# Kernel optimization log

Measured on AMD Instinct MI355X. Metric: run time of the kernel, lower is better.

Reference implementation:

```python
import jax, jax.numpy as jnp
import numpy as np

H = 8  # attention heads
L = 2  # transformer layers


def conv1d(x, w, b=None, pad=0, dil=1):
    # x: (B, Cin, T), w: (Cout, Cin, K)
    y = jax.lax.conv_general_dilated(x, w, window_strides=(1,), padding=[(pad, pad)],
                                     rhs_dilation=(dil,), dimension_numbers=('NCH', 'OIH', 'NCH'))
    if b is not None:
        y = y + b[None, :, None]
    return y


def bn1d(x, p, eps=1e-5):
    # eval-mode BatchNorm1d; p: (4, C) = [gamma, beta, running_mean, running_var]
    g, b, m, v = p
    return g[None, :, None] * (x - m[None, :, None]) * jax.lax.rsqrt(v + eps)[None, :, None] + b[None, :, None]


def layernorm(x, g, b, eps=1e-5):
    m = x.mean(-1, keepdims=True)
    v = ((x - m) ** 2).mean(-1, keepdims=True)
    return (x - m) * jax.lax.rsqrt(v + eps) * g + b


def mha(x, in_w, in_b, out_w, out_b):
    # x: (T, B, E) seq-first, like nn.MultiheadAttention (eval, no dropout)
    T, B, E = x.shape
    dh = E // H
    qkv = x @ in_w.T + in_b
    q, k, v = jnp.split(qkv, 3, axis=-1)
    sh = lambda a: a.reshape(T, B, H, dh).transpose(1, 2, 0, 3)  # (B, H, T, dh)
    q, k, v = sh(q), sh(k), sh(v)
    attn = jax.nn.softmax(jnp.einsum('bhqd,bhkd->bhqk', q, k) * (dh ** -0.5), axis=-1)
    o = jnp.einsum('bhqk,bhkd->bhqd', attn, v).transpose(2, 0, 1, 3).reshape(T, B, E)
    return o @ out_w.T + out_b


def _forward(x, wts, cw1, cb1, bn1, cw2, cb2, bn2, cw3, cb3, bn3, cw4, cb4, bn4, cw5,
             tcw_in, tcb_in, t_in_w, t_in_b, t_out_w, t_out_b, ln1_g, ln1_b,
             ff_w1, ff_b1, ff_w2, ff_b2, ln2_g, ln2_b, tcw_out, tcb_out,
             cw6, bn6, bw1, bb1, bw2, bb2, bw3, bb3):
    out = x.transpose(0, 2, 1)  # (B, 2048, T)
    residual = out
    # multi-dilation conv branches: Conv1d -> ReLU -> BN
    o1 = bn1d(jax.nn.relu(conv1d(out, cw1, cb1, pad=1)), bn1)
    o2 = bn1d(jax.nn.relu(conv1d(out, cw2, cb2, pad=2, dil=2)), bn2)
    o3 = bn1d(jax.nn.relu(conv1d(out, cw3, cb3, pad=4, dil=4)), bn3)
    o4 = bn1d(jax.nn.relu(conv1d(out, cw4, cb4, pad=8, dil=4)), bn4)  # k=5, d=4, p=8
    out_d = wts[0] * o1 + wts[1] * o2 + wts[2] * o3 + wts[3] * o4  # (B, 512, T)
    # conv_5: 2048 -> 512, k=1, no bias
    out = jax.nn.relu(conv1d(out, cw5))
    # TransformerFeatureAggregator
    out = conv1d(out, tcw_in, tcb_in)  # 1x1 conv 512->512
    out = out.transpose(2, 0, 1)  # (T, B, 512)
    for i in range(L):
        a = mha(out, t_in_w[i], t_in_b[i], t_out_w[i], t_out_b[i])
        out = layernorm(out + a, ln1_g[i], ln1_b[i])
        ff = jax.nn.relu(out @ ff_w1[i].T + ff_b1[i]) @ ff_w2[i].T + ff_b2[i]
        out = layernorm(out + ff, ln2_g[i], ln2_b[i])
    out = out.transpose(1, 2, 0)  # (B, 512, T)
    out = conv1d(out, tcw_out, tcb_out)
    out = jnp.concatenate([out_d, out], axis=1)  # (B, 1024, T)
    out = bn1d(jax.nn.relu(conv1d(out, cw6, pad=1)), bn6)  # (B, 2048, T)
    # Bottleneck residual block
    r = out
    b = jax.nn.relu(conv1d(out, bw1, bb1))
    b = jax.nn.relu(conv1d(b, bw2, bb2, pad=1))
    b = conv1d(b, bw3, bb3)
    out = jax.nn.relu(b + r)
    out = out + residual
    return out.transpose(0, 2, 1)  # (B, T, 2048)


def setup_inputs() -> dict:
    key = jax.random.key(0)
    ks = iter(jax.random.split(key, 80))

    def rn(shape, s=0.02):
        return jax.random.normal(next(ks), shape, jnp.float32) * s

    def bn_p(c):
        return jnp.stack([1.0 + rn((c,), 0.1), rn((c,), 0.1), rn((c,), 0.1),
                          0.5 + jax.random.uniform(next(ks), (c,), jnp.float32)])

    B, T, D = 8, 1024, 2048
    return dict(
        x=jax.random.normal(next(ks), (B, T, D), jnp.float32),
        wts=jnp.ones((4,), jnp.float32),
        cw1=rn((512, D, 3)), cb1=rn((512,)), bn1=bn_p(512),
        cw2=rn((512, D, 3)), cb2=rn((512,)), bn2=bn_p(512),
        cw3=rn((512, D, 3)), cb3=rn((512,)), bn3=bn_p(512),
        cw4=rn((512, D, 5)), cb4=rn((512,)), bn4=bn_p(512),
        cw5=rn((512, D, 1)),
        tcw_in=rn((512, 512, 1)), tcb_in=rn((512,)),
        t_in_w=rn((L, 3 * 512, 512)), t_in_b=rn((L, 3 * 512)),
        t_out_w=rn((L, 512, 512)), t_out_b=rn((L, 512)),
        ln1_g=jnp.ones((L, 512), jnp.float32), ln1_b=jnp.zeros((L, 512), jnp.float32),
        ff_w1=rn((L, 2048, 512)), ff_b1=rn((L, 2048)),
        ff_w2=rn((L, 512, 2048)), ff_b2=rn((L, 512)),
        ln2_g=jnp.ones((L, 512), jnp.float32), ln2_b=jnp.zeros((L, 512), jnp.float32),
        tcw_out=rn((512, 512, 1)), tcb_out=rn((512,)),
        cw6=rn((2048, 1024, 3)), bn6=bn_p(2048),
        bw1=rn((512, 2048, 1)), bb1=rn((512,)),
        bw2=rn((512, 512, 3)), bb2=rn((512,)),
        bw3=rn((2048, 512, 1)), bb3=rn((2048,)),
    )


def reference(x, wts, cw1, cb1, bn1, cw2, cb2, bn2, cw3, cb3, bn3, cw4, cb4, bn4, cw5,
              tcw_in, tcb_in, t_in_w, t_in_b, t_out_w, t_out_b, ln1_g, ln1_b,
              ff_w1, ff_b1, ff_w2, ff_b2, ln2_g, ln2_b, tcw_out, tcb_out,
              cw6, bn6, bw1, bb1, bw2, bb2, bw3, bb3):
    return _forward(x, wts, cw1, cb1, bn1, cw2, cb2, bn2, cw3, cb3, bn3, cw4, cb4, bn4, cw5,
                    tcw_in, tcb_in, t_in_w, t_in_b, t_out_w, t_out_b, ln1_g, ln1_b,
                    ff_w1, ff_b1, ff_w2, ff_b2, ln2_g, ln2_b, tcw_out, tcb_out,
                    cw6, bn6, bw1, bb1, bw2, bb2, bw3, bb3)
```

## Files before the change

### kernel.cpp

```cpp
#include <hip/hip_runtime.h>
#include <hip/hip_bf16.h>


typedef __attribute__((ext_vector_type(4))) float f32x4;
typedef __attribute__((ext_vector_type(8))) short short8;
typedef __attribute__((ext_vector_type(8))) unsigned short ushort8;

__device__ __forceinline__ unsigned short f2bu(float f) {
    __hip_bfloat16 h = __float2bfloat16(f);
    return *reinterpret_cast<unsigned short*>(&h);
}
__device__ __forceinline__ float bu2f(unsigned short u) {
    __hip_bfloat16 h = *reinterpret_cast<__hip_bfloat16*>(&u);
    return __bfloat162float(h);
}

__device__ __forceinline__ void gload16(const void* g, void* l) {
    __builtin_amdgcn_global_load_lds(
        (const __attribute__((address_space(1))) unsigned int*)g,
        (__attribute__((address_space(3))) unsigned int*)l, 16, 0, 0);
}

__global__ void cast_kernel(const float* __restrict__ in, unsigned short* __restrict__ out, int n8)
{
    for (int i = blockIdx.x * blockDim.x + threadIdx.x; i < n8; i += gridDim.x * blockDim.x) {
        const float4* p = (const float4*)in + (size_t)i * 2;
        float4 a = p[0], b = p[1];
        ushort8 o;
        o[0] = f2bu(a.x); o[1] = f2bu(a.y); o[2] = f2bu(a.z); o[3] = f2bu(a.w);
        o[4] = f2bu(b.x); o[5] = f2bu(b.y); o[6] = f2bu(b.z); o[7] = f2bu(b.w);
        *(ushort8*)(out + (size_t)i * 8) = o;
    }
}

struct WJob { const float* src; unsigned short* dst; int N, K, taps; };
struct WJobs { WJob j[14]; int n; };

__global__ void wtrans_multi(WJobs jobs)
{
    for (int q = 0; q < jobs.n; ++q) {
        const float* __restrict__ src = jobs.j[q].src;
        unsigned short* __restrict__ dst = jobs.j[q].dst;
        const int N = jobs.j[q].N, K = jobs.j[q].K, taps = jobs.j[q].taps;
        const int total = N * K * taps;
        for (int idx = blockIdx.x * blockDim.x + threadIdx.x; idx < total;
             idx += gridDim.x * blockDim.x) {
            int i   = idx % K;
            int rem = idx / K;
            int o   = rem % N;
            int k   = rem / N;
            dst[idx] = f2bu(src[((size_t)o * K + i) * (size_t)taps + k]);
        }
    }
}

#define SKEY(r) (((r) >> 2) & 3)

template<int BM_, int EPI>
__global__ __launch_bounds__(256)
void mgemm(const __hip_bfloat16* __restrict__ A, int lda,
           const __hip_bfloat16* __restrict__ Bw, const float* __restrict__ bias,
           float* __restrict__ Cf, __hip_bfloat16* __restrict__ Cb, int ldc,
           int N, int K,
           const float* __restrict__ r1, int ldr, const float* __restrict__ r2)
{
    constexpr int MREP = BM_ / 32;
    __shared__ __align__(16) short As[2][BM_ * 32];
    __shared__ __align__(16) short Bs[2][128 * 32];

    const int tid  = threadIdx.x;
    const int w    = tid >> 6;
    const int lane = tid & 63;
    const int wr   = w >> 1, wc = w & 1;
    const int m_base = blockIdx.x * BM_;
    const int n_base = blockIdx.y * 128;
    const int lrr = lane >> 2;
    const int lj  = lane & 3;

    f32x4 acc[MREP][4];
#pragma unroll
    for (int m = 0; m < MREP; ++m)
#pragma unroll
        for (int n = 0; n < 4; ++n) acc[m][n] = (f32x4){0.f, 0.f, 0.f, 0.f};

    auto stage = [&](int nb, int kc) {
#pragma unroll
        for (int cb = 0; cb < 2; ++cb) {
            const int cc = w + cb * 4;
            const int r  = cc * 16 + lrr;
            const int jc = lj ^ SKEY(r);
            gload16((const void*)(Bw + (size_t)(n_base + r) * K + kc + jc * 8),
                    (void*)&Bs[nb][cc * 512]);
        }
#pragma unroll
        for (int ca = 0; ca < BM_ / 64; ++ca) {
            const int cc = w + ca * 4;
            const int r  = cc * 16 + lrr;
            const int jc = lj ^ SKEY(r);
            gload16((const void*)(A + (size_t)(m_base + r) * lda + kc + jc * 8),
                    (void*)&As[nb][cc * 512]);
        }
    };

    stage(0, 0);
    __syncthreads();
    int cur = 0;
    const int nt = K / 32;
    for (int t = 0; t < nt; ++t) {
        if (t + 1 < nt) stage(cur ^ 1, (t + 1) * 32);

        short8 a[MREP], b[4];
#pragma unroll
        for (int m = 0; m < MREP; ++m) {
            const int i = wr * (BM_ / 2) + m * 16 + (lane & 15);
            a[m] = *(const short8*)&As[cur][i * 32 + (((lane >> 4) ^ SKEY(i)) * 8)];
        }
#pragma unroll
        for (int n = 0; n < 4; ++n) {
            const int r = wc * 64 + n * 16 + (lane & 15);
            b[n] = *(const short8*)&Bs[cur][r * 32 + (((lane >> 4) ^ SKEY(r)) * 8)];
        }
#pragma unroll
        for (int m = 0; m < MREP; ++m)
#pragma unroll
            for (int n = 0; n < 4; ++n)
                acc[m][n] = __builtin_amdgcn_mfma_f32_16x16x32_bf16(a[m], b[n], acc[m][n], 0, 0, 0);

        __syncthreads();
        cur ^= 1;
    }

#pragma unroll
    for (int m = 0; m < MREP; ++m) {
#pragma unroll
        for (int n = 0; n < 4; ++n) {
#pragma unroll
            for (int j = 0; j < 4; ++j) {
                const int row = m_base + wr * (BM_ / 2) + m * 16 + (lane >> 4) * 4 + j;
                const int col = n_base + wc * 64 + n * 16 + (lane & 15);
                float v = acc[m][n][j];
                if (bias) v += bias[col];
                const size_t idx = (size_t)row * ldc + col;
                if (EPI == 1) v = fmaxf(v, 0.f);
                if (EPI == 3) {
                    v += r1[(size_t)row * ldr + col];
                    v = fmaxf(v, 0.f) + r2[(size_t)row * 2048 + col];
                    Cf[idx] = v;
                } else {
                    if (Cf) Cf[idx] = v;
                    if (Cb) Cb[idx] = __float2bfloat16(v);
                }
            }
        }
    }
}

template<int NTAPS, int EPI>
__global__ __launch_bounds__(256)
void cgemm(const __hip_bfloat16* __restrict__ A1, const __hip_bfloat16* __restrict__ A2,
           int split, int lda,
           const __hip_bfloat16* __restrict__ Bw, const float* __restrict__ bias,
           float* __restrict__ Cf, __hip_bfloat16* __restrict__ Cb, int ldc,
           int N, int K,
           int o0, int o1, int o2,
           const float* __restrict__ bnp,
           const __hip_bfloat16* __restrict__ zb)
{
    __shared__ __align__(16) short As[144 * 32];
    __shared__ __align__(16) short Bs[NTAPS * 128 * 32];

    const int tid  = threadIdx.x;
    const int w    = tid >> 6;
    const int lane = tid & 63;
    const int wr   = w >> 1, wc = w & 1;
    const int m_base = blockIdx.x * 128;
    const int n_base = blockIdx.y * 128;
    const int tb   = m_base & 1023;
    const int lrr  = lane >> 2;
    const int lj   = lane & 3;

    f32x4 acc[4][4];
#pragma unroll
    for (int m = 0; m < 4; ++m)
#pragma unroll
        for (int n = 0; n < 4; ++n) acc[m][n] = (f32x4){0.f, 0.f, 0.f, 0.f};

    for (int kc = 0; kc < K; kc += 32) {
        __syncthreads();
        for (int c = w; c < 9; c += 4) {
            const int i    = c * 16 + lrr;
            const int jc   = lj ^ SKEY(i);
            const int trow = tb + i - 8;
            const int c0   = kc + jc * 8;
            const void* src;
            if ((unsigned)trow < 1024u) {
                const int g = m_base - 8 + i;
                src = (c0 < split) ? (const void*)(A1 + (size_t)g * lda + c0)
                                   : (const void*)(A2 + (size_t)g * lda + (c0 - split));
            } else {
                src = (const void*)(zb + jc * 8);
            }
            gload16(src, (void*)&As[c * 512]);
        }
        for (int cb = w; cb < NTAPS * 8; cb += 4) {
            const int tap = cb >> 3, sub = cb & 7;
            const int r   = sub * 16 + lrr;
            const int jc  = lj ^ SKEY(r);
            gload16((const void*)(Bw + ((size_t)tap * N + n_base + r) * K + kc + jc * 8),
                    (void*)&Bs[cb * 512]);
        }
        __syncthreads();

#pragma unroll
        for (int tap = 0; tap < NTAPS; ++tap) {
            const int off = (tap == 0) ? o0 : (tap == 1) ? o1 : o2;
            short8 a[4], b[4];
#pragma unroll
            for (int m = 0; m < 4; ++m) {
                const int i = 8 + off + wr * 64 + m * 16 + (lane & 15);
                a[m] = *(const short8*)&As[i * 32 + (((lane >> 4) ^ SKEY(i)) * 8)];
            }
#pragma unroll
            for (int n = 0; n < 4; ++n) {
                const int r = wc * 64 + n * 16 + (lane & 15);
                b[n] = *(const short8*)&Bs[tap * 4096 + r * 32 + (((lane >> 4) ^ SKEY(r)) * 8)];
            }
#pragma unroll
            for (int m = 0; m < 4; ++m)
#pragma unroll
                for (int n = 0; n < 4; ++n)
                    acc[m][n] = __builtin_amdgcn_mfma_f32_16x16x32_bf16(a[m], b[n], acc[m][n], 0, 0, 0);
        }
    }

#pragma unroll
    for (int m = 0; m < 4; ++m) {
#pragma unroll
        for (int n = 0; n < 4; ++n) {
#pragma unroll
            for (int j = 0; j < 4; ++j) {
                const int row = m_base + wr * 64 + m * 16 + (lane >> 4) * 4 + j;
                const int col = n_base + wc * 64 + n * 16 + (lane & 15);
                float v = acc[m][n][j];
                if (bias) v += bias[col];
                const size_t idx = (size_t)row * ldc + col;
                if (EPI == 1) v = fmaxf(v, 0.f);
                if (EPI == 2) {
                    v = fmaxf(v, 0.f);
                    const float g  = bnp[col];
                    const float be = bnp[N + col];
                    const float mu = bnp[2 * N + col];
                    const float va = bnp[3 * N + col];
                    v = g * (v - mu) * rsqrtf(va + 1e-5f) + be;
                }
                if (Cf) Cf[idx] = v;
                if (Cb) Cb[idx] = __float2bfloat16(v);
            }
        }
    }
}

template<int NTAPS>
__global__ __launch_bounds__(512, 4)
void cgemm2(const __hip_bfloat16* __restrict__ A1, const __hip_bfloat16* __restrict__ A2,
            int split, int lda,
            const __hip_bfloat16* __restrict__ Bw, const float* __restrict__ bias,
            float* __restrict__ Cf, __hip_bfloat16* __restrict__ Cb, int ldc,
            int N, int K,
            int o0, int o1, int o2,
            const float* __restrict__ bnp,
            const __hip_bfloat16* __restrict__ zb)
{
    __shared__ __align__(16) short As[272 * 32];
    __shared__ __align__(16) short Bs[NTAPS * 128 * 32];

    const int tid  = threadIdx.x;
    const int w    = tid >> 6;
    const int lane = tid & 63;
    const int wr   = w >> 1, wc = w & 1;
    const int m_base = blockIdx.x * 256;
    const int n_base = blockIdx.y * 128;
    const int tb   = m_base & 1023;
    const int lrr  = lane >> 2;
    const int lj   = lane & 3;

    f32x4 acc[4][4];
#pragma unroll
    for (int m = 0; m < 4; ++m)
#pragma unroll
        for (int n = 0; n < 4; ++n) acc[m][n] = (f32x4){0.f, 0.f, 0.f, 0.f};

    for (int kc = 0; kc < K; kc += 32) {
        __syncthreads();
        for (int c = w; c < 17; c += 8) {
            const int i    = c * 16 + lrr;
            const int jc   = lj ^ SKEY(i);
            const int trow = tb + i - 8;
            const int c0   = kc + jc * 8;
            const void* src;
            if ((unsigned)trow < 1024u) {
                const int g = m_base - 8 + i;
                src = (c0 < split) ? (const void*)(A1 + (size_t)g * lda + c0)
                                   : (const void*)(A2 + (size_t)g * lda + (c0 - split));
            } else {
                src = (const void*)(zb + jc * 8);
            }
            gload16(src, (void*)&As[c * 512]);
        }
        for (int cb = w; cb < NTAPS * 8; cb += 8) {
            const int tap = cb >> 3, sub = cb & 7;
            const int r   = sub * 16 + lrr;
            const int jc  = lj ^ SKEY(r);
            gload16((const void*)(Bw + ((size_t)tap * N + n_base + r) * K + kc + jc * 8),
                    (void*)&Bs[cb * 512]);
        }
        __syncthreads();

#pragma unroll
        for (int tap = 0; tap < NTAPS; ++tap) {
            const int off = (tap == 0) ? o0 : (tap == 1) ? o1 : o2;
            short8 a[4], b[4];
#pragma unroll
            for (int m = 0; m < 4; ++m) {
                const int i = 8 + off + wr * 64 + m * 16 + (lane & 15);
                a[m] = *(const short8*)&As[i * 32 + (((lane >> 4) ^ SKEY(i)) * 8)];
            }
#pragma unroll
            for (int n = 0; n < 4; ++n) {
                const int r = wc * 64 + n * 16 + (lane & 15);
                b[n] = *(const short8*)&Bs[tap * 4096 + r * 32 + (((lane >> 4) ^ SKEY(r)) * 8)];
            }
#pragma unroll
            for (int m = 0; m < 4; ++m)
#pragma unroll
                for (int n = 0; n < 4; ++n)
                    acc[m][n] = __builtin_amdgcn_mfma_f32_16x16x32_bf16(a[m], b[n], acc[m][n], 0, 0, 0);
        }
    }

#pragma unroll
    for (int m = 0; m < 4; ++m) {
#pragma unroll
        for (int n = 0; n < 4; ++n) {
#pragma unroll
            for (int j = 0; j < 4; ++j) {
                const int row = m_base + wr * 64 + m * 16 + (lane >> 4) * 4 + j;
                const int col = n_base + wc * 64 + n * 16 + (lane & 15);
                float v = acc[m][n][j];
                if (bias) v += bias[col];
                v = fmaxf(v, 0.f);
                const float g  = bnp[col];
                const float be = bnp[N + col];
                const float mu = bnp[2 * N + col];
                const float va = bnp[3 * N + col];
                v = g * (v - mu) * rsqrtf(va + 1e-5f) + be;
                const size_t idx = (size_t)row * ldc + col;
                if (Cf) Cf[idx] = v;
                if (Cb) Cb[idx] = __float2bfloat16(v);
            }
        }
    }
}

struct BrP {
    const __hip_bfloat16* W;
    const float* bias;
    const float* bn;
    __hip_bfloat16* out;
    int ntaps;
    int o0, o1, o2, o3, o4;
};
struct BrPs { BrP p[5]; };

__global__ __launch_bounds__(512, 4)
void bgemm(const __hip_bfloat16* __restrict__ A, BrPs ps,
           const float* __restrict__ wts,
           const __hip_bfloat16* __restrict__ zb)
{
    __shared__ __align__(16) short As[272 * 32];
    __shared__ __align__(16) short Bs[5 * 128 * 32];

    const int tid  = threadIdx.x;
    const int w    = tid >> 6;
    const int lane = tid & 63;
    const int wr   = w >> 1, wc = w & 1;
    const int m_base = blockIdx.x * 256;
    const int n_base = blockIdx.y * 128;
    const int z    = blockIdx.z;
    const BrP p    = ps.p[z];
    const int tb   = m_base & 1023;
    const int lrr  = lane >> 2;
    const int lj   = lane & 3;
    const int ntaps = p.ntaps;

    f32x4 acc[4][4];
#pragma unroll
    for (int m = 0; m < 4; ++m)
#pragma unroll
        for (int n = 0; n < 4; ++n) acc[m][n] = (f32x4){0.f, 0.f, 0.f, 0.f};

    for (int kc = 0; kc < 2048; kc += 32) {
        __syncthreads();
        for (int c = w; c < 17; c += 8) {
            const int i    = c * 16 + lrr;
            const int jc   = lj ^ SKEY(i);
            const int trow = tb + i - 8;
            const void* src;
            if ((unsigned)trow < 1024u)
                src = (const void*)(A + (size_t)(m_base - 8 + i) * 2048 + kc + jc * 8);
            else
                src = (const void*)(zb + jc * 8);
            gload16(src, (void*)&As[c * 512]);
        }
        for (int cb = w; cb < ntaps * 8; cb += 8) {
            const int tap = cb >> 3, sub = cb & 7;
            const int r   = sub * 16 + lrr;
            const int jc  = lj ^ SKEY(r);
            gload16((const void*)(p.W + ((size_t)tap * 512 + n_base + r) * 2048 + kc + jc * 8),
                    (void*)&Bs[cb * 512]);
        }
        __syncthreads();

#pragma unroll 5
        for (int tap = 0; tap < ntaps; ++tap) {
            const int off = (tap == 0) ? p.o0 : (tap == 1) ? p.o1 : (tap == 2) ? p.o2
                          : (tap == 3) ? p.o3 : p.o4;
            short8 a[4], b[4];
#pragma unroll
            for (int m = 0; m < 4; ++m) {
                const int i = 8 + off + wr * 64 + m * 16 + (lane & 15);
                a[m] = *(const short8*)&As[i * 32 + (((lane >> 4) ^ SKEY(i)) * 8)];
            }
#pragma unroll
            for (int n = 0; n < 4; ++n) {
                const int r = wc * 64 + n * 16 + (lane & 15);
                b[n] = *(const short8*)&Bs[tap * 4096 + r * 32 + (((lane >> 4) ^ SKEY(r)) * 8)];
            }
#pragma unroll
            for (int m = 0; m < 4; ++m)
#pragma unroll
                for (int n = 0; n < 4; ++n)
                    acc[m][n] = __builtin_amdgcn_mfma_f32_16x16x32_bf16(a[m], b[n], acc[m][n], 0, 0, 0);
        }
    }

    const float wz = wts[z & 3];
#pragma unroll
    for (int m = 0; m < 4; ++m) {
#pragma unroll
        for (int n = 0; n < 4; ++n) {
#pragma unroll
            for (int j = 0; j < 4; ++j) {
                const int row = m_base + wr * 64 + m * 16 + (lane >> 4) * 4 + j;
                const int col = n_base + wc * 64 + n * 16 + (lane & 15);
                float v = acc[m][n][j];
                if (p.bias) v += p.bias[col];
                v = fmaxf(v, 0.f);
                if (p.bn) {
                    const float g  = p.bn[col];
                    const float be = p.bn[512 + col];
                    const float mu = p.bn[1024 + col];
                    const float va = p.bn[1536 + col];
                    v = (g * (v - mu) * rsqrtf(va + 1e-5f) + be) * wz;
                }
                p.out[(size_t)row * 512 + col] = __float2bfloat16(v);
            }
        }
    }
}

__global__ void bsum_kernel(const unsigned short* __restrict__ b0, const unsigned short* __restrict__ b1,
                            const unsigned short* __restrict__ b2, const unsigned short* __restrict__ b3,
                            unsigned short* __restrict__ o, int n8)
{
    for (int i = blockIdx.x * blockDim.x + threadIdx.x; i < n8; i += gridDim.x * blockDim.x) {
        ushort8 v0 = *(const ushort8*)(b0 + (size_t)i * 8);
        ushort8 v1 = *(const ushort8*)(b1 + (size_t)i * 8);
        ushort8 v2 = *(const ushort8*)(b2 + (size_t)i * 8);
        ushort8 v3 = *(const ushort8*)(b3 + (size_t)i * 8);
        ushort8 r;
#pragma unroll
        for (int e = 0; e < 8; ++e)
            r[e] = f2bu(bu2f(v0[e]) + bu2f(v1[e]) + bu2f(v2[e]) + bu2f(v3[e]));
        *(ushort8*)(o + (size_t)i * 8) = r;
    }
}

__global__ __launch_bounds__(256)
void ln_kernel(float* __restrict__ x, const float* __restrict__ t,
               const float* __restrict__ g, const float* __restrict__ b,
               __hip_bfloat16* __restrict__ xb, int M)
{
    const int wave = threadIdx.x >> 6;
    const int lane = threadIdx.x & 63;
    const int row  = blockIdx.x * 4 + wave;
    if (row >= M) return;
    float* xr = x + (size_t)row * 512;
    const float* tr = t + (size_t)row * 512;
    float v[8];
    float s = 0.f, s2 = 0.f;
#pragma unroll
    for (int j = 0; j < 8; ++j) {
        float val = xr[lane * 8 + j] + tr[lane * 8 + j];
        v[j] = val; s += val; s2 += val * val;
    }
#pragma unroll
    for (int d = 1; d < 64; d <<= 1) {
        s  += __shfl_xor(s, d, 64);
        s2 += __shfl_xor(s2, d, 64);
    }
    const float mean = s * (1.f / 512.f);
    const float var  = s2 * (1.f / 512.f) - mean * mean;
    const float rstd = rsqrtf(var + 1e-5f);
#pragma unroll
    for (int j = 0; j < 8; ++j) {
        const int c = lane * 8 + j;
        const float o = (v[j] - mean) * rstd * g[c] + b[c];
        xr[c] = o;
        xb[(size_t)row * 512 + c] = __float2bfloat16(o);
    }
}

__global__ __launch_bounds__(256)
void mattn(const __hip_bfloat16* __restrict__ qkv, __hip_bfloat16* __restrict__ o)
{
    __shared__ __align__(16) short Ks[4096];
    __shared__ __align__(16) short Vt[4096];
    __shared__ __align__(16) short Pl[8192];

    const int tid  = threadIdx.x;
    const int w    = tid >> 6;
    const int lane = tid & 63;
    const int g    = lane >> 4;
    const int li   = lane & 15;
    const int b    = blockIdx.x >> 3;
    const int h    = blockIdx.x & 7;
    const int qb   = blockIdx.y * 128 + w * 32;

    const short* qkvs = (const short*)qkv;

    short8 qf[2][2];
#pragma unroll
    for (int m = 0; m < 2; ++m)
#pragma unroll
        for (int ks = 0; ks < 2; ++ks)
            qf[m][ks] = *(const short8*)(qkvs +
                (size_t)(b * 1024 + qb + m * 16 + li) * 1536 + h * 64 + ks * 32 + g * 8);

    f32x4 Oa[2][4];
    float mr[2][4], lr[2][4];
#pragma unroll
    for (int m = 0; m < 2; ++m)
#pragma unroll
        for (int j = 0; j < 4; ++j) { mr[m][j] = -1e30f; lr[m][j] = 0.f; }
#pragma unroll
    for (int m = 0; m < 2; ++m)
#pragma unroll
        for (int n = 0; n < 4; ++n) Oa[m][n] = (f32x4){0.f, 0.f, 0.f, 0.f};

    const int sr = tid >> 2;
    const int sc = (tid & 3) * 16;

    for (int kt = 0; kt < 16; ++kt) {
        __syncthreads();
        const short* kr = qkvs + (size_t)(b * 1024 + kt * 64 + sr) * 1536 + 512 + h * 64 + sc;
        short8 k0 = *(const short8*)kr;
        short8 k1 = *(const short8*)(kr + 8);
        short8 v0 = *(const short8*)(kr + 512);
        short8 v1 = *(const short8*)(kr + 520);
        const int swr = (sr & 7) << 4;
        *(short8*)&Ks[(sr * 128 + ((sc * 2) ^ swr)) >> 1] = k0;
        *(short8*)&Ks[(sr * 128 + ((sc * 2 + 16) ^ swr)) >> 1] = k1;
#pragma unroll
        for (int e = 0; e < 8; ++e) {
            const int d = sc + e;
            Vt[(d * 128 + ((sr * 2) ^ ((d & 7) << 4))) >> 1] = v0[e];
        }
#pragma unroll
        for (int e = 0; e < 8; ++e) {
            const int d = sc + 8 + e;
            Vt[(d * 128 + ((sr * 2) ^ ((d & 7) << 4))) >> 1] = v1[e];
        }
        __syncthreads();

        short8 kf[4][2], vf[4][2];
#pragma unroll
        for (int n = 0; n < 4; ++n) {
            const int r  = n * 16 + li;
            const int sw = (r & 7) << 4;
#pragma unroll
            for (int ks = 0; ks < 2; ++ks) {
                const int cb = ks * 64 + g * 16;
                kf[n][ks] = *(const short8*)&Ks[(r * 128 + (cb ^ sw)) >> 1];
                vf[n][ks] = *(const short8*)&Vt[(r * 128 + (cb ^ sw)) >> 1];
            }
        }

        f32x4 s[2][4];
#pragma unroll
        for (int m = 0; m < 2; ++m)
#pragma unroll
            for (int n = 0; n < 4; ++n) s[m][n] = (f32x4){0.f, 0.f, 0.f, 0.f};
#pragma unroll
        for (int m = 0; m < 2; ++m)
#pragma unroll
            for (int n = 0; n < 4; ++n)
#pragma unroll
                for (int ks = 0; ks < 2; ++ks)
                    s[m][n] = __builtin_amdgcn_mfma_f32_16x16x32_bf16(qf[m][ks], kf[n][ks], s[m][n], 0, 0, 0);

#pragma unroll
        for (int m = 0; m < 2; ++m) {
            float cc[4];
#pragma unroll
            for (int j = 0; j < 4; ++j) {
                float rm = fmaxf(fmaxf(s[m][0][j], s[m][1][j]), fmaxf(s[m][2][j], s[m][3][j]));
                rm *= 0.125f;
#pragma unroll
                for (int d = 1; d < 16; d <<= 1) rm = fmaxf(rm, __shfl_xor(rm, d, 64));
                const float mn = fmaxf(mr[m][j], rm);
                cc[j] = __expf(mr[m][j] - mn);
                mr[m][j] = mn;
            }
            float rs[4] = {0.f, 0.f, 0.f, 0.f};
#pragma unroll
            for (int n = 0; n < 4; ++n)
#pragma unroll
                for (int j = 0; j < 4; ++j) {
                    const float pv = __expf(s[m][n][j] * 0.125f - mr[m][j]);
                    rs[j] += pv;
                    const int r  = m * 16 + g * 4 + j;
                    const int cb = (n * 16 + li) * 2;
                    Pl[(w * 4096 + r * 128 + (cb ^ ((r & 7) << 4))) >> 1] = (short)f2bu(pv);
                }
#pragma unroll
            for (int j = 0; j < 4; ++j) {
#pragma unroll
                for (int d = 1; d < 16; d <<= 1) rs[j] += __shfl_xor(rs[j], d, 64);
                lr[m][j] = lr[m][j] * cc[j] + rs[j];
#pragma unroll
                for (int n = 0; n < 4; ++n) Oa[m][n][j] *= cc[j];
            }
        }
        __syncthreads();

        short8 pa[2][2];
#pragma unroll
        for (int m = 0; m < 2; ++m) {
            const int r  = m * 16 + li;
            const int sw = (r & 7) << 4;
#pragma unroll
            for (int ks = 0; ks < 2; ++ks) {
                const int cb = ks * 64 + g * 16;
                pa[m][ks] = *(const short8*)&Pl[(w * 4096 + r * 128 + (cb ^ sw)) >> 1];
            }
        }
#pragma unroll
        for (int m = 0; m < 2; ++m)
#pragma unroll
            for (int n = 0; n < 4; ++n)
#pragma unroll
                for (int ks = 0; ks < 2; ++ks)
                    Oa[m][n] = __builtin_amdgcn_mfma_f32_16x16x32_bf16(pa[m][ks], vf[n][ks], Oa[m][n], 0, 0, 0);
    }

#pragma unroll
    for (int m = 0; m < 2; ++m)
#pragma unroll
        for (int j = 0; j < 4; ++j) {
            const float inv = 1.f / lr[m][j];
            const size_t row = (size_t)(b * 1024 + qb + m * 16 + g * 4 + j);
#pragma unroll
            for (int n = 0; n < 4; ++n)
                o[row * 512 + h * 64 + n * 16 + li] = __float2bfloat16(Oa[m][n][j] * inv);
        }
}


extern "C" void kernel_launch(void* const* d_in, const int* in_sizes, int n_in,
                              void* d_out, int out_size, void* d_ws, size_t ws_size,
                              hipStream_t stream)
{
    const float* x       = (const float*)d_in[0];
    const float* wts     = (const float*)d_in[1];
    const float* cw1     = (const float*)d_in[2];
    const float* cb1     = (const float*)d_in[3];
    const float* bn1     = (const float*)d_in[4];
    const float* cw2     = (const float*)d_in[5];
    const float* cb2     = (const float*)d_in[6];
    const float* bn2     = (const float*)d_in[7];
    const float* cw3     = (const float*)d_in[8];
    const float* cb3     = (const float*)d_in[9];
    const float* bn3     = (const float*)d_in[10];
    const float* cw4     = (const float*)d_in[11];
    const float* cb4     = (const float*)d_in[12];
    const float* bn4     = (const float*)d_in[13];
    const float* cw5     = (const float*)d_in[14];
    const float* tcw_in  = (const float*)d_in[15];
    const float* tcb_in  = (const float*)d_in[16];
    const float* t_in_w  = (const float*)d_in[17];
    const float* t_in_b  = (const float*)d_in[18];
    const float* t_out_w = (const float*)d_in[19];
    const float* t_out_b = (const float*)d_in[20];
    const float* ln1_g   = (const float*)d_in[21];
    const float* ln1_b   = (const float*)d_in[22];
    const float* ff_w1   = (const float*)d_in[23];
    const float* ff_b1   = (const float*)d_in[24];
    const float* ff_w2   = (const float*)d_in[25];
    const float* ff_b2   = (const float*)d_in[26];
    const float* ln2_g   = (const float*)d_in[27];
    const float* ln2_b   = (const float*)d_in[28];
    const float* tcw_out = (const float*)d_in[29];
    const float* tcb_out = (const float*)d_in[30];
    const float* cw6     = (const float*)d_in[31];
    const float* bn6     = (const float*)d_in[32];
    const float* bw1     = (const float*)d_in[33];
    const float* bb1     = (const float*)d_in[34];
    const float* bw2     = (const float*)d_in[35];
    const float* bb2     = (const float*)d_in[36];
    const float* bw3     = (const float*)d_in[37];
    const float* bb3     = (const float*)d_in[38];
    float* out = (float*)d_out;

    const size_t HMB = 524288;
    char* ws = (char*)d_ws;
    auto BF = [&](double mb) { return (__hip_bfloat16*)(ws + (size_t)(mb * 2) * HMB); };
    auto FP = [&](double mb) { return (float*)(ws + (size_t)(mb * 2) * HMB); };

    __hip_bfloat16* xb    = BF(0);
    float*          h7    = FP(0);
    __hip_bfloat16* bigqb = BF(32);
    __hip_bfloat16* wc1   = BF(32);
    __hip_bfloat16* wc2   = BF(39);
    __hip_bfloat16* wc3   = BF(46);
    __hip_bfloat16* wc4   = BF(53);
    __hip_bfloat16* wc5   = BF(64);
    __hip_bfloat16* wti0  = BF(66.5);
    __hip_bfloat16* wti1  = BF(68);
    __hip_bfloat16* wto0  = BF(69.5);
    __hip_bfloat16* wto1  = BF(70);
    __hip_bfloat16* wf10  = BF(70.5);
    __hip_bfloat16* wf11  = BF(72.5);
    __hip_bfloat16* wf20  = BF(74.5);
    __hip_bfloat16* wf21  = BF(76.5);
    __hip_bfloat16* wtci  = BF(78.5);
    __hip_bfloat16* wtco  = BF(79);
    __hip_bfloat16* bigb  = BF(80);
    __hip_bfloat16* h7b   = BF(80);
    __hip_bfloat16* br0   = BF(112);
    __hip_bfloat16* br1   = BF(120);
    __hip_bfloat16* br2   = BF(128);
    __hip_bfloat16* br3   = BF(136);
    float*          tmp   = FP(112);
    float*          xtf   = FP(128);
    __hip_bfloat16* outdb = BF(144);
    __hip_bfloat16* wc6   = BF(152);
    __hip_bfloat16* wtb1  = BF(165);
    __hip_bfloat16* wtb2  = BF(167.5);
    __hip_bfloat16* wtb3  = BF(169);
    __hip_bfloat16* tmpb  = BF(171);
    __hip_bfloat16* atnb  = BF(171);
    __hip_bfloat16* xtfb  = BF(179);
    __hip_bfloat16* zb    = BF(188);

    const int M = 8192;
    dim3 blk(256);
    dim3 blk2(512);

    auto mg = [&](int bm, int epi, const __hip_bfloat16* A, int lda,
                  const __hip_bfloat16* Bw, const float* bias,
                  float* Cf, __hip_bfloat16* Cb, int ldc, int N, int K,
                  const float* r1, int ldr, const float* r2) {
        dim3 grid(M / bm, N / 128);
#define LAU(BMV, EPIV) mgemm<BMV, EPIV><<<grid, blk, 0, stream>>>(A, lda, Bw, bias, Cf, Cb, ldc, N, K, r1, ldr, r2)
        if (bm == 64) {
            switch (epi) { case 0: LAU(64, 0); break; case 1: LAU(64, 1); break;
                           default: LAU(64, 3); }
        } else {
            switch (epi) { case 0: LAU(128, 0); break; case 1: LAU(128, 1); break;
                           default: LAU(128, 3); }
        }
#undef LAU
    };

    hipMemsetAsync(zb, 0, 8192, stream);
    cast_kernel<<<dim3(2048), blk, 0, stream>>>(x, (unsigned short*)xb, M * 2048 / 8);

    WJobs early{};
    early.n = 5;
    early.j[0] = {cw1, (unsigned short*)wc1, 512, 2048, 3};
    early.j[1] = {cw2, (unsigned short*)wc2, 512, 2048, 3};
    early.j[2] = {cw3, (unsigned short*)wc3, 512, 2048, 3};
    early.j[3] = {cw4, (unsigned short*)wc4, 512, 2048, 5};
    early.j[4] = {cw5, (unsigned short*)wc5, 512, 2048, 1};
    wtrans_multi<<<dim3(2048), blk, 0, stream>>>(early);

    WJobs pers{};
    pers.n = 14;
    pers.j[0]  = {t_in_w,                (unsigned short*)wti0, 1536, 512, 1};
    pers.j[1]  = {t_in_w + 1536 * 512,   (unsigned short*)wti1, 1536, 512, 1};
    pers.j[2]  = {t_out_w,               (unsigned short*)wto0, 512, 512, 1};
    pers.j[3]  = {t_out_w + 512 * 512,   (unsigned short*)wto1, 512, 512, 1};
    pers.j[4]  = {ff_w1,                 (unsigned short*)wf10, 2048, 512, 1};
    pers.j[5]  = {ff_w1 + 2048 * 512,    (unsigned short*)wf11, 2048, 512, 1};
    pers.j[6]  = {ff_w2,                 (unsigned short*)wf20, 512, 2048, 1};
    pers.j[7]  = {ff_w2 + 512 * 2048,    (unsigned short*)wf21, 512, 2048, 1};
    pers.j[8]  = {tcw_in,                (unsigned short*)wtci, 512, 512, 1};
    pers.j[9]  = {tcw_out,               (unsigned short*)wtco, 512, 512, 1};
    pers.j[10] = {cw6,                   (unsigned short*)wc6, 2048, 1024, 3};
    pers.j[11] = {bw1,                   (unsigned short*)wtb1, 512, 2048, 1};
    pers.j[12] = {bw2,                   (unsigned short*)wtb2, 512, 512, 3};
    pers.j[13] = {bw3,                   (unsigned short*)wtb3, 2048, 512, 1};
    wtrans_multi<<<dim3(2048), blk, 0, stream>>>(pers);

    BrPs bp{};
    bp.p[0] = {wc1, cb1, bn1, br0, 3, -1, 0, 1, 0, 0};
    bp.p[1] = {wc2, cb2, bn2, br1, 3, -2, 0, 2, 0, 0};
    bp.p[2] = {wc3, cb3, bn3, br2, 3, -4, 0, 4, 0, 0};
    bp.p[3] = {wc4, cb4, bn4, br3, 5, -8, -4, 0, 4, 8};
    bp.p[4] = {wc5, nullptr, nullptr, tmpb, 1, 0, 0, 0, 0, 0};
    bgemm<<<dim3(M / 256, 4, 5), blk2, 0, stream>>>(xb, bp, wts, zb);
    bsum_kernel<<<dim3(2048), blk, 0, stream>>>((const unsigned short*)br0, (const unsigned short*)br1,
                                                (const unsigned short*)br2, (const unsigned short*)br3,
                                                (unsigned short*)outdb, M * 512 / 8);

    mg(64, 0, tmpb, 512, wtci, tcb_in, xtf, xtfb, 512, 512, 512, nullptr, 0, nullptr);

    for (int l = 0; l < 2; ++l) {
        const __hip_bfloat16* wi = l ? wti1 : wti0;
        const __hip_bfloat16* wo = l ? wto1 : wto0;
        const __hip_bfloat16* w1 = l ? wf11 : wf10;
        const __hip_bfloat16* w2 = l ? wf21 : wf20;
        mg(128, 0, xtfb, 512, wi, t_in_b + l * 1536, nullptr, bigqb, 1536, 1536, 512,
           nullptr, 0, nullptr);
        mattn<<<dim3(64, 8), blk, 0, stream>>>(bigqb, atnb);
        mg(64, 0, atnb, 512, wo, t_out_b + l * 512, tmp, nullptr, 512, 512, 512,
           nullptr, 0, nullptr);
        ln_kernel<<<dim3(M / 4), blk, 0, stream>>>(xtf, tmp, ln1_g + l * 512, ln1_b + l * 512, xtfb, M);
        mg(128, 1, xtfb, 512, w1, ff_b1 + l * 2048, nullptr, bigb, 2048, 2048, 512,
           nullptr, 0, nullptr);
        mg(64, 0, bigb, 2048, w2, ff_b2 + l * 512, tmp, nullptr, 512, 512, 2048,
           nullptr, 0, nullptr);
        ln_kernel<<<dim3(M / 4), blk, 0, stream>>>(xtf, tmp, ln2_g + l * 512, ln2_b + l * 512, xtfb, M);
    }

    mg(64, 0, xtfb, 512, wtco, tcb_out, nullptr, atnb, 512, 512, 512, nullptr, 0, nullptr);

    cgemm2<3><<<dim3(M / 256, 16), blk2, 0, stream>>>(outdb, atnb, 512, 512, wc6, nullptr,
        h7, h7b, 2048, 2048, 1024, -1, 0, 1, bn6, zb);

    mg(64, 1, h7b, 2048, wtb1, bb1, nullptr, outdb, 512, 512, 2048, nullptr, 0, nullptr);
    cgemm<3, 1><<<dim3(M / 128, 4), blk, 0, stream>>>(outdb, outdb, 4096, 512, wtb2, bb2,
        nullptr, tmpb, 512, 512, 512, -1, 0, 1, nullptr, zb);
    mg(128, 3, tmpb, 512, wtb3, bb3, out, nullptr, 2048, 2048, 512, h7, 2048, x);

    (void)in_sizes; (void)n_in; (void)out_size; (void)ws_size;
}
```

Measured before the change: 1.164 ms.

## Add 256x128 double-buffered GEMM for wide projections and split branch conv launch

Adds a new pgemm kernel that uses 512-thread blocks with 256x128 output tiles and double-buffered async global-to-LDS loads. It is used for the QKV projection, FF1 and the final bottleneck GEMM in place of the 128-row mgemm. The aim is more operand reuse per block and fewer blocks for these large-N GEMMs. The multi-branch conv launch is also split into a 3-tap and a 5/1-tap launch, so the 3-tap branches allocate less shared memory for B and can reach higher occupancy. The trade-offs are fewer blocks in the grid, which may underfill the GPU, and one extra kernel launch.

Result: slower. 1.199 ms (+3.1%).

```diff
diff --git a/kernel.cpp b/kernel.cpp
--- a/kernel.cpp
+++ b/kernel.cpp
@@ -137,6 +137,102 @@
 #pragma unroll
             for (int j = 0; j < 4; ++j) {
                 const int row = m_base + wr * (BM_ / 2) + m * 16 + (lane >> 4) * 4 + j;
+                const int col = n_base + wc * 64 + n * 16 + (lane & 15);
+                float v = acc[m][n][j];
+                if (bias) v += bias[col];
+                const size_t idx = (size_t)row * ldc + col;
+                if (EPI == 1) v = fmaxf(v, 0.f);
+                if (EPI == 3) {
+                    v += r1[(size_t)row * ldr + col];
+                    v = fmaxf(v, 0.f) + r2[(size_t)row * 2048 + col];
+                    Cf[idx] = v;
+                } else {
+                    if (Cf) Cf[idx] = v;
+                    if (Cb) Cb[idx] = __float2bfloat16(v);
+                }
+            }
+        }
+    }
+}
+
+template<int EPI>
+__global__ __launch_bounds__(512, 4)
+void pgemm(const __hip_bfloat16* __restrict__ A, int lda,
+           const __hip_bfloat16* __restrict__ Bw, const float* __restrict__ bias,
+           float* __restrict__ Cf, __hip_bfloat16* __restrict__ Cb, int ldc,
+           int N, int K,
+           const float* __restrict__ r1, int ldr, const float* __restrict__ r2)
+{
+    __shared__ __align__(16) short As[2][256 * 32];
+    __shared__ __align__(16) short Bs[2][128 * 32];
+
+    const int tid  = threadIdx.x;
+    const int w    = tid >> 6;
+    const int lane = tid & 63;
+    const int wr   = w >> 1, wc = w & 1;
+    const int m_base = blockIdx.x * 256;
+    const int n_base = blockIdx.y * 128;
+    const int lrr = lane >> 2;
+    const int lj  = lane & 3;
+
+    f32x4 acc[4][4];
+#pragma unroll
+    for (int m = 0; m < 4; ++m)
+#pragma unroll
+        for (int n = 0; n < 4; ++n) acc[m][n] = (f32x4){0.f, 0.f, 0.f, 0.f};
+
+    auto stage = [&](int nb, int kc) {
+        {
+            const int r  = w * 16 + lrr;
+            const int jc = lj ^ SKEY(r);
+            gload16((const void*)(Bw + (size_t)(n_base + r) * K + kc + jc * 8),
+                    (void*)&Bs[nb][w * 512]);
+        }
+#pragma unroll
+        for (int ca = 0; ca < 2; ++ca) {
+            const int cc = w + ca * 8;
+            const int r  = cc * 16 + lrr;
+            const int jc = lj ^ SKEY(r);
+            gload16((const void*)(A + (size_t)(m_base + r) * lda + kc + jc * 8),
+                    (void*)&As[nb][cc * 512]);
+        }
+    };
+
+    stage(0, 0);
+    __syncthreads();
+    int cur = 0;
+    const int nt = K / 32;
+    for (int t = 0; t < nt; ++t) {
+        if (t + 1 < nt) stage(cur ^ 1, (t + 1) * 32);
+
+        short8 a[4], b[4];
+#pragma unroll
+        for (int m = 0; m < 4; ++m) {
+            const int i = wr * 64 + m * 16 + (lane & 15);
+            a[m] = *(const short8*)&As[cur][i * 32 + (((lane >> 4) ^ SKEY(i)) * 8)];
+        }
+#pragma unroll
+        for (int n = 0; n < 4; ++n) {
+            const int r = wc * 64 + n * 16 + (lane & 15);
+            b[n] = *(const short8*)&Bs[cur][r * 32 + (((lane >> 4) ^ SKEY(r)) * 8)];
+        }
+#pragma unroll
+        for (int m = 0; m < 4; ++m)
+#pragma unroll
+            for (int n = 0; n < 4; ++n)
+                acc[m][n] = __builtin_amdgcn_mfma_f32_16x16x32_bf16(a[m], b[n], acc[m][n], 0, 0, 0);
+
+        __syncthreads();
+        cur ^= 1;
+    }
+
+#pragma unroll
+    for (int m = 0; m < 4; ++m) {
+#pragma unroll
+        for (int n = 0; n < 4; ++n) {
+#pragma unroll
+            for (int j = 0; j < 4; ++j) {
+                const int row = m_base + wr * 64 + m * 16 + (lane >> 4) * 4 + j;
                 const int col = n_base + wc * 64 + n * 16 + (lane & 15);
                 float v = acc[m][n][j];
                 if (bias) v += bias[col];
@@ -367,18 +463,19 @@
     const float* bias;
     const float* bn;
     __hip_bfloat16* out;
-    int ntaps;
+    int ntaps, wti;
     int o0, o1, o2, o3, o4;
 };
-struct BrPs { BrP p[5]; };
-
+struct BrPs { BrP p[3]; };
+
+template<int NT>
 __global__ __launch_bounds__(512, 4)
 void bgemm(const __hip_bfloat16* __restrict__ A, BrPs ps,
            const float* __restrict__ wts,
            const __hip_bfloat16* __restrict__ zb)
 {
     __shared__ __align__(16) short As[272 * 32];
-    __shared__ __align__(16) short Bs[5 * 128 * 32];
+    __shared__ __align__(16) short Bs[NT * 128 * 32];
 
     const int tid  = threadIdx.x;
     const int w    = tid >> 6;
@@ -444,7 +541,7 @@
         }
     }
 
-    const float wz = wts[z & 3];
+    const float wz = wts[p.wti];
 #pragma unroll
     for (int m = 0; m < 4; ++m) {
 #pragma unroll
@@ -783,6 +880,18 @@
 #undef LAU
     };
 
+    auto pg = [&](int epi, const __hip_bfloat16* A, int lda,
+                  const __hip_bfloat16* Bw, const float* bias,
+                  float* Cf, __hip_bfloat16* Cb, int ldc, int N, int K,
+                  const float* r1, int ldr, const float* r2) {
+        dim3 grid(M / 256, N / 128);
+        switch (epi) {
+        case 0: pgemm<0><<<grid, blk2, 0, stream>>>(A, lda, Bw, bias, Cf, Cb, ldc, N, K, r1, ldr, r2); break;
+        case 1: pgemm<1><<<grid, blk2, 0, stream>>>(A, lda, Bw, bias, Cf, Cb, ldc, N, K, r1, ldr, r2); break;
+        default: pgemm<3><<<grid, blk2, 0, stream>>>(A, lda, Bw, bias, Cf, Cb, ldc, N, K, r1, ldr, r2); break;
+        }
+    };
+
     hipMemsetAsync(zb, 0, 8192, stream);
     cast_kernel<<<dim3(2048), blk, 0, stream>>>(x, (unsigned short*)xb, M * 2048 / 8);
 
@@ -813,13 +922,15 @@
     pers.j[13] = {bw3,                   (unsigned short*)wtb3, 2048, 512, 1};
     wtrans_multi<<<dim3(2048), blk, 0, stream>>>(pers);
 
-    BrPs bp{};
-    bp.p[0] = {wc1, cb1, bn1, br0, 3, -1, 0, 1, 0, 0};
-    bp.p[1] = {wc2, cb2, bn2, br1, 3, -2, 0, 2, 0, 0};
-    bp.p[2] = {wc3, cb3, bn3, br2, 3, -4, 0, 4, 0, 0};
-    bp.p[3] = {wc4, cb4, bn4, br3, 5, -8, -4, 0, 4, 8};
-    bp.p[4] = {wc5, nullptr, nullptr, tmpb, 1, 0, 0, 0, 0, 0};
-    bgemm<<<dim3(M / 256, 4, 5), blk2, 0, stream>>>(xb, bp, wts, zb);
+    BrPs bp3{};
+    bp3.p[0] = {wc1, cb1, bn1, br0, 3, 0, -1, 0, 1, 0, 0};
+    bp3.p[1] = {wc2, cb2, bn2, br1, 3, 1, -2, 0, 2, 0, 0};
+    bp3.p[2] = {wc3, cb3, bn3, br2, 3, 2, -4, 0, 4, 0, 0};
+    bgemm<3><<<dim3(M / 256, 4, 3), blk2, 0, stream>>>(xb, bp3, wts, zb);
+    BrPs bp5{};
+    bp5.p[0] = {wc4, cb4, bn4, br3, 5, 3, -8, -4, 0, 4, 8};
+    bp5.p[1] = {wc5, nullptr, nullptr, tmpb, 1, 0, 0, 0, 0, 0, 0};
+    bgemm<5><<<dim3(M / 256, 4, 2), blk2, 0, stream>>>(xb, bp5, wts, zb);
     bsum_kernel<<<dim3(2048), blk, 0, stream>>>((const unsigned short*)br0, (const unsigned short*)br1,
                                                 (const unsigned short*)br2, (const unsigned short*)br3,
                                                 (unsigned short*)outdb, M * 512 / 8);
@@ -831,13 +942,13 @@
         const __hip_bfloat16* wo = l ? wto1 : wto0;
         const __hip_bfloat16* w1 = l ? wf11 : wf10;
         const __hip_bfloat16* w2 = l ? wf21 : wf20;
-        mg(128, 0, xtfb, 512, wi, t_in_b + l * 1536, nullptr, bigqb, 1536, 1536, 512,
+        pg(0, xtfb, 512, wi, t_in_b + l * 1536, nullptr, bigqb, 1536, 1536, 512,
            nullptr, 0, nullptr);
         mattn<<<dim3(64, 8), blk, 0, stream>>>(bigqb, atnb);
         mg(64, 0, atnb, 512, wo, t_out_b + l * 512, tmp, nullptr, 512, 512, 512,
            nullptr, 0, nullptr);
         ln_kernel<<<dim3(M / 4), blk, 0, stream>>>(xtf, tmp, ln1_g + l * 512, ln1_b + l * 512, xtfb, M);
-        mg(128, 1, xtfb, 512, w1, ff_b1 + l * 2048, nullptr, bigb, 2048, 2048, 512,
+        pg(1, xtfb, 512, w1, ff_b1 + l * 2048, nullptr, bigb, 2048, 2048, 512,
            nullptr, 0, nullptr);
         mg(64, 0, bigb, 2048, w2, ff_b2 + l * 512, tmp, nullptr, 512, 512, 2048,
            nullptr, 0, nullptr);
@@ -852,7 +963,7 @@
     mg(64, 1, h7b, 2048, wtb1, bb1, nullptr, outdb, 512, 512, 2048, nullptr, 0, nullptr);
     cgemm<3, 1><<<dim3(M / 128, 4), blk, 0, stream>>>(outdb, outdb, 4096, 512, wtb2, bb2,
         nullptr, tmpb, 512, 512, 512, -1, 0, 1, nullptr, zb);
-    mg(128, 3, tmpb, 512, wtb3, bb3, out, nullptr, 2048, 2048, 512, h7, 2048, x);
+    pg(3, tmpb, 512, wtb3, bb3, out, nullptr, 2048, 2048, 512, h7, 2048, x);
 
     (void)in_sizes; (void)n_in; (void)out_size; (void)ws_size;
 }
```
